# Optimization experiments

Hardware: AMD Instinct MI355X
Metric: run time of the kernel (lower is better)

The kernel has to match this reference:

```python
import jax, jax.numpy as jnp
import numpy as np
from math import factorial

# irreps: list of (multiplicity, l, parity) -- "128x0e + 64x1o + 32x2e"
IRREPS = [(128, 0, 1), (64, 1, -1), (32, 2, 1)]


def _change_basis_real_to_complex(l):
    # e3nn convention: complex SH basis expressed in terms of real SH basis
    q = np.zeros((2 * l + 1, 2 * l + 1), dtype=np.complex128)
    for m in range(-l, 0):
        q[l + m, l + abs(m)] = 1 / np.sqrt(2)
        q[l + m, l - abs(m)] = -1j / np.sqrt(2)
    q[l, l] = 1
    for m in range(1, l + 1):
        q[l + m, l + abs(m)] = (-1) ** m / np.sqrt(2)
        q[l + m, l - abs(m)] = 1j * (-1) ** m / np.sqrt(2)
    return (-1j) ** l * q  # phase makes the real CG coefficients real


def _su2_cg(j1, j2, j3):
    f = factorial
    C = np.zeros((2 * j1 + 1, 2 * j2 + 1, 2 * j3 + 1))
    for m1 in range(-j1, j1 + 1):
        for m2 in range(-j2, j2 + 1):
            m3 = m1 + m2
            if abs(m3) > j3:
                continue
            pref = ((2 * j3 + 1) * f(j3 + j1 - j2) * f(j3 - j1 + j2) * f(j1 + j2 - j3) / f(j1 + j2 + j3 + 1)
                    * f(j3 + m3) * f(j3 - m3) * f(j1 - m1) * f(j1 + m1) * f(j2 - m2) * f(j2 + m2)) ** 0.5
            s = 0.0
            for k in range(0, j1 + j2 - j3 + 1):
                if j1 - m1 - k < 0 or j2 + m2 - k < 0 or j3 - j2 + m1 + k < 0 or j3 - j1 - m2 + k < 0:
                    continue
                s += (-1) ** k / (f(k) * f(j1 + j2 - j3 - k) * f(j1 - m1 - k) * f(j2 + m2 - k)
                                  * f(j3 - j2 + m1 + k) * f(j3 - j1 - m2 + k))
            C[j1 + m1, j2 + m2, j3 + m3] = pref * s
    return C


def _real_cg(l1, l2, l3):
    # real (Wigner-3j style) CG, normalized so sum of squares == 1
    Q1 = _change_basis_real_to_complex(l1)
    Q2 = _change_basis_real_to_complex(l2)
    Q3 = _change_basis_real_to_complex(l3)
    C = _su2_cg(l1, l2, l3).astype(np.complex128)
    C = np.einsum('ij,kl,mn,ikm->jln', Q1, Q2, Q3, C).real
    return (C / np.linalg.norm(C)).astype(np.float32)


def _build_paths():
    paths, fan_in, woff = [], [0] * len(IRREPS), 0
    for i1, (m1, l1, p1) in enumerate(IRREPS):
        for i2, (m2, l2, p2) in enumerate(IRREPS):
            for i3, (m3, l3, p3) in enumerate(IRREPS):
                if p1 * p2 != p3 or not (abs(l1 - l2) <= l3 <= l1 + l2):
                    continue
                paths.append((i1, i2, i3, woff, _real_cg(l1, l2, l3)))
                woff += m1 * m2 * m3
                fan_in[i3] += m1 * m2
    return paths, fan_in, woff

PATHS, FAN_IN, WEIGHT_NUMEL = _build_paths()  # WEIGHT_NUMEL == 4489216
OFFS = np.cumsum([0] + [m * (2 * l + 1) for m, l, _ in IRREPS])  # block offsets (mul_ir layout)
BATCH = 8192


def setup_inputs() -> dict:
    key = jax.random.key(0)
    k1, k2, k3 = jax.random.split(key, 3)
    x1 = jax.random.normal(k1, (BATCH, int(OFFS[-1])), dtype=jnp.float32)
    x2 = jax.random.normal(k2, (BATCH, int(OFFS[-1])), dtype=jnp.float32)
    weight = jax.random.normal(k3, (WEIGHT_NUMEL,), dtype=jnp.float32)
    return {"x1": x1, "x2": x2, "weight": weight}


def reference(x1, x2, weight):
    b = x1.shape[0]
    out_blocks = [jnp.zeros((b, m, 2 * l + 1), dtype=x1.dtype) for m, l, _ in IRREPS]
    for i1, i2, i3, wo, cg in PATHS:
        m1, l1, _ = IRREPS[i1]
        m2, l2, _ = IRREPS[i2]
        m3, l3, _ = IRREPS[i3]
        W = weight[wo:wo + m1 * m2 * m3].reshape(m1, m2, m3)
        xb1 = x1[:, OFFS[i1]:OFFS[i1 + 1]].reshape(b, m1, 2 * l1 + 1)
        xb2 = x2[:, OFFS[i2]:OFFS[i2 + 1]].reshape(b, m2, 2 * l2 + 1)
        # component irrep-norm + element path-norm: sqrt(dim_out / fan_in)
        coeff = np.sqrt((2 * l3 + 1) / FAN_IN[i3]).astype(np.float32)
        out_blocks[i3] = out_blocks[i3] + coeff * jnp.einsum(
            'uvw,bui,bvj,ijk->bwk', W, xb1, xb2, jnp.asarray(cg))
    return jnp.concatenate([ob.reshape(b, -1) for ob in out_blocks], axis=1)
```

## Files before the change

### kernel.cpp

```cpp
#include <hip/hip_runtime.h>
#include <math.h>

#define DIMX 480

typedef float v4f __attribute__((ext_vector_type(4)));
typedef __bf16 v8bf __attribute__((ext_vector_type(8)));
typedef __bf16 v4bf __attribute__((ext_vector_type(4)));

__constant__ int c_pl[11][3] = {
    {0,0,0},{0,1,1},{0,2,2},{1,0,1},{1,1,0},{1,1,2},
    {1,2,1},{2,0,2},{2,1,1},{2,2,0},{2,2,2}};
__constant__ int c_cgoff[11] = {0,1,10,35,44,53,98,143,168,213,238};
__constant__ int c_order[11] = {8,5,0,3,10,4,7,9,6,1,2};

struct cplx { double re, im; };
__device__ inline cplx cmul(cplx a, cplx b) {
    return { a.re*b.re - a.im*b.im, a.re*b.im + a.im*b.re };
}
__device__ double dfact(int n) { double r = 1.0; for (int i = 2; i <= n; ++i) r *= (double)i; return r; }

__device__ double su2cg_elem(int j1, int j2, int j3, int m1, int m2) {
    int m3 = m1 + m2;
    if (m3 < -j3 || m3 > j3) return 0.0;
    double pref = (2.0*j3 + 1.0)
        * dfact(j3 + j1 - j2) * dfact(j3 - j1 + j2) * dfact(j1 + j2 - j3)
        / dfact(j1 + j2 + j3 + 1)
        * dfact(j3 + m3) * dfact(j3 - m3) * dfact(j1 - m1) * dfact(j1 + m1)
        * dfact(j2 - m2) * dfact(j2 + m2);
    pref = sqrt(pref);
    double s = 0.0;
    for (int k = 0; k <= j1 + j2 - j3; ++k) {
        if (j1 - m1 - k < 0 || j2 + m2 - k < 0 ||
            j3 - j2 + m1 + k < 0 || j3 - j1 - m2 + k < 0) continue;
        double d = dfact(k) * dfact(j1 + j2 - j3 - k) * dfact(j1 - m1 - k)
                 * dfact(j2 + m2 - k) * dfact(j3 - j2 + m1 + k) * dfact(j3 - j1 - m2 + k);
        s += ((k & 1) ? -1.0 : 1.0) / d;
    }
    return pref * s;
}

__device__ cplx Qval(int l, int mi, int ri) {
    const double is2 = 0.70710678118654752440;
    int m = mi - l;
    cplx q = {0.0, 0.0};
    if (m < 0) {
        if (ri == l - m)       q = { is2, 0.0 };
        else if (ri == l + m)  q = { 0.0, -is2 };
    } else if (m == 0) {
        if (ri == l)           q = { 1.0, 0.0 };
    } else {
        double s = (m & 1) ? -1.0 : 1.0;
        if (ri == l + m)       q = { s * is2, 0.0 };
        else if (ri == l - m)  q = { 0.0, s * is2 };
    }
    int ph = l & 3;
    cplx r;
    if (ph == 0)      r = q;
    else if (ph == 1) r = {  q.im, -q.re };
    else if (ph == 2) r = { -q.re, -q.im };
    else              r = { -q.im,  q.re };
    return r;
}

__global__ void cg_init_kernel(float* __restrict__ cgout) {
    int p = blockIdx.x;
    int l1 = c_pl[p][0], l2 = c_pl[p][1], l3 = c_pl[p][2];
    int D2 = 2*l2 + 1, D3 = 2*l3 + 1;
    int D = (2*l1 + 1) * D2 * D3;
    int e = threadIdx.x;
    double val = 0.0;
    if (e < D) {
        int j  = e / (D2 * D3);
        int l_ = (e / D3) % D2;
        int n  = e % D3;
        for (int m1 = -l1; m1 <= l1; ++m1)
            for (int m2 = -l2; m2 <= l2; ++m2) {
                int m3 = m1 + m2;
                if (m3 < -l3 || m3 > l3) continue;
                double cgv = su2cg_elem(l1, l2, l3, m1, m2);
                if (cgv == 0.0) continue;
                cplx t = cmul(cmul(Qval(l1, l1 + m1, j), Qval(l2, l2 + m2, l_)),
                              Qval(l3, l3 + m3, n));
                val += t.re * cgv;
            }
    }
    __shared__ double sh[128];
    sh[threadIdx.x] = val * val;
    __syncthreads();
    for (int s = 64; s > 0; s >>= 1) {
        if (threadIdx.x < s) sh[threadIdx.x] += sh[threadIdx.x + s];
        __syncthreads();
    }
    double nrm = sqrt(sh[0]);
    if (e < D) cgout[c_cgoff[p] + e] = (float)(val / nrm);
}

__global__ __launch_bounds__(256) void wt2_kernel(const float* __restrict__ w,
                                                  __bf16* __restrict__ wt2) {
    int c = blockIdx.x * 256 + threadIdx.x;
    int sec, cc;
    if (c < 344064)      { sec = 0; cc = c; }
    else if (c < 507904) { sec = 1; cc = c - 344064; }
    else                 { sec = 2; cc = c - 507904; }
    int l = cc & 15, quad = (cc >> 4) & 3;
    int nblk, kblk, N; size_t soff;
    if (sec == 0)      { nblk = (cc >> 6) & 7; kblk = cc >> 9; N = 128; soff = 0; }
    else if (sec == 1) { nblk = (cc >> 6) & 3; kblk = cc >> 8; N = 64;  soff = 2752512; }
    else               { nblk = (cc >> 6) & 1; kblk = cc >> 7; N = 32;  soff = 4063232; }
    int n = nblk * 16 + l;
    int k = kblk * 32 + quad * 8;
    int rb, pb;
    if (sec == 0) {
        if (k < 16384)      { rb = 0;     pb = 0; }
        else if (k < 20480) { rb = 16384; pb = 3276800; }
        else                { rb = 20480; pb = 4325376; }
    } else if (sec == 1) {
        if (k < 8192)       { rb = 0;     pb = 2097152; }
        else if (k < 16384) { rb = 8192;  pb = 2752512; }
        else if (k < 18432) { rb = 16384; pb = 3932160; }
        else                { rb = 18432; pb = 4194304; }
    } else {
        if (k < 4096)       { rb = 0;     pb = 2621440; }
        else if (k < 8192)  { rb = 4096;  pb = 3801088; }
        else if (k < 12288) { rb = 8192;  pb = 4063232; }
        else                { rb = 12288; pb = 4456448; }
    }
    const float* src = w + pb + (size_t)(k - rb) * N + n;
    v8bf o;
    #pragma unroll
    for (int j = 0; j < 8; ++j) o[j] = (__bf16)src[(size_t)j * N];
    *(v8bf*)(&wt2[soff + (size_t)cc * 8]) = o;
}

static __device__ __forceinline__ void stage_tile(const float* __restrict__ x,
        int b0, int c0, int n4, int S, __bf16* __restrict__ d, int tid) {
    const int cnt = 32 * n4;
    for (int c = tid; c < cnt; c += 256) {
        int row = c / n4, ch = c - row * n4;
        float4 v = *(const float4*)(x + (size_t)(b0 + row) * DIMX + c0 + ch * 4);
        v4bf p;
        p[0] = (__bf16)v.x; p[1] = (__bf16)v.y; p[2] = (__bf16)v.z; p[3] = (__bf16)v.w;
        *(v4bf*)(&d[row * S + ch * 4]) = p;
    }
}

#define XE(A, i) ((float)A[(i) >> 3][(i) & 7])

#define PAIR_REDUCE(NA)                                                  \
    {                                                                    \
        v4f* red_ = (v4f*)xs;                                            \
        __syncthreads();                                                 \
        if (kh) {                                                        \
            _Pragma("unroll")                                            \
            for (int a_ = 0; a_ < (NA); ++a_)                            \
                red_[(rt * 64 + lane) * (NA) + a_] = acc[a_];            \
        }                                                                \
        __syncthreads();                                                 \
        if (!kh) {                                                       \
            _Pragma("unroll")                                            \
            for (int a_ = 0; a_ < (NA); ++a_)                            \
                acc[a_] += red_[(rt * 64 + lane) * (NA) + a_];           \
        }                                                                \
    }

__global__ __launch_bounds__(256, 4) void tp_path(
    const float* __restrict__ x1, const float* __restrict__ x2,
    const __bf16* __restrict__ wt2, const float* __restrict__ cg,
    float* __restrict__ out, float* __restrict__ pa,
    float* __restrict__ pb, float* __restrict__ pc)
{
    __shared__ __align__(16) __bf16 xs[12800];
    const int tid  = threadIdx.x;
    const int lane = tid & 63;
    const int wv   = tid >> 6;
    const int quad = lane >> 4;
    const int l16  = lane & 15;
    const int rt   = wv & 1;
    const int kh   = wv >> 1;
    const int path = c_order[blockIdx.x >> 8];
    const int b0   = (blockIdx.x & 255) * 32;
    const int qil  = (quad * 16 + l16) * 8;
    const int lrow = rt * 16 + l16;

    const float c0n = sqrtf(1.0f / 21504.0f);
    const float c1n = sqrtf(3.0f / 20480.0f);
    const float c2n = sqrtf(5.0f / 13312.0f);

    switch (path) {
    case 0: {
        const int S = 136;
        stage_tile(x1, b0, 0, 32, S, xs, tid);
        stage_tile(x2, b0, 0, 32, S, xs + 32*S, tid);
        __syncthreads();
        const __bf16* X1L = xs + lrow * S;
        const __bf16* X2L = xs + 32*S + lrow * S;
        const float s0 = cg[0] * c0n;
        v4f acc[8];
        #pragma unroll
        for (int c = 0; c < 8; ++c) acc[c] = (v4f)0.f;
        #pragma unroll 1
        for (int u = kh*64; u < kh*64 + 64; ++u) {
            const float s = s0 * (float)X1L[u];
            #pragma unroll 1
            for (int q4 = 0; q4 < 4; ++q4) {
                v8bf xv = *(const v8bf*)(X2L + 32*q4 + quad * 8);
                v8bf af;
                #pragma unroll
                for (int j = 0; j < 8; ++j) af[j] = (__bf16)(s * (float)xv[j]);
                const __bf16* bp = wt2 + (size_t)((u*4 + q4) * 8) * 512 + qil;
                #pragma unroll
                for (int ct = 0; ct < 8; ++ct) {
                    v8bf bf = *(const v8bf*)(bp + ct * 512);
                    acc[ct] = __builtin_amdgcn_mfma_f32_16x16x32_bf16(af, bf, acc[ct], 0, 0, 0);
                }
            }
        }
        PAIR_REDUCE(8)
        if (!kh) {
            #pragma unroll
            for (int i = 0; i < 4; ++i) {
                int r = b0 + rt*16 + quad*4 + i;
                #pragma unroll
                for (int ct = 0; ct < 8; ++ct)
                    out[(size_t)r * DIMX + ct*16 + l16] = acc[ct][i];
            }
        }
        break; }
    case 1: {
        const int S = 200;
        stage_tile(x1, b0, 128, 48, S, xs, tid);
        stage_tile(x2, b0, 128, 48, S, xs + 32*S, tid);
        __syncthreads();
        const __bf16* X1L = xs + lrow * S;
        const __bf16* X2L = xs + 32*S + lrow * S;
        const float d0 = cg[44]*c0n, d1 = cg[48]*c0n, d2 = cg[52]*c0n;
        v4f acc[8];
        #pragma unroll
        for (int c = 0; c < 8; ++c) acc[c] = (v4f)0.f;
        #pragma unroll 1
        for (int tu = kh*32; tu < kh*32 + 32; ++tu) {
            const int u3 = 3 * tu;
            const float m0 = d0*(float)X1L[u3], m1 = d1*(float)X1L[u3+1], m2 = d2*(float)X1L[u3+2];
            #pragma unroll 1
            for (int h = 0; h < 2; ++h) {
                const int col = 96*h + 24*quad;
                v8bf a[3];
                a[0] = *(const v8bf*)(X2L + col);
                a[1] = *(const v8bf*)(X2L + col + 8);
                a[2] = *(const v8bf*)(X2L + col + 16);
                v8bf af;
                #pragma unroll
                for (int j = 0; j < 8; ++j)
                    af[j] = (__bf16)(m0*XE(a,3*j) + m1*XE(a,3*j+1) + m2*XE(a,3*j+2));
                const __bf16* bp = wt2 + (size_t)((512 + tu*2 + h) * 8) * 512 + qil;
                #pragma unroll
                for (int ct = 0; ct < 8; ++ct) {
                    v8bf bf = *(const v8bf*)(bp + ct * 512);
                    acc[ct] = __builtin_amdgcn_mfma_f32_16x16x32_bf16(af, bf, acc[ct], 0, 0, 0);
                }
            }
        }
        PAIR_REDUCE(8)
        if (!kh) {
            #pragma unroll
            for (int i = 0; i < 4; ++i) {
                int r = b0 + rt*16 + quad*4 + i;
                #pragma unroll
                for (int ct = 0; ct < 8; ++ct)
                    pa[(size_t)r * DIMX + ct*16 + l16] = acc[ct][i];
            }
        }
        break; }
    case 2: {
        const int S = 168;
        stage_tile(x1, b0, 320, 40, S, xs, tid);
        stage_tile(x2, b0, 320, 40, S, xs + 32*S, tid);
        __syncthreads();
        const __bf16* X1L = xs + lrow * S;
        const __bf16* X2L = xs + 32*S + lrow * S;
        v4f acc[8];
        #pragma unroll
        for (int c = 0; c < 8; ++c) acc[c] = (v4f)0.f;
        v8bf a[5];
        #pragma unroll
        for (int q = 0; q < 5; ++q) a[q] = *(const v8bf*)(X2L + 40*quad + 8*q);
        #pragma unroll 1
        for (int t = kh*16; t < kh*16 + 16; ++t) {
            const int u5 = 5 * t;
            float m[5];
            #pragma unroll
            for (int kk = 0; kk < 5; ++kk) m[kk] = cg[213+6*kk]*c0n*(float)X1L[u5+kk];
            v8bf af;
            #pragma unroll
            for (int j = 0; j < 8; ++j) {
                float s = 0.f;
                #pragma unroll
                for (int kk = 0; kk < 5; ++kk) s += m[kk] * XE(a, 5*j+kk);
                af[j] = (__bf16)s;
            }
            const __bf16* bp = wt2 + (size_t)((640+t) * 8) * 512 + qil;
            #pragma unroll
            for (int ct = 0; ct < 8; ++ct) {
                v8bf bf = *(const v8bf*)(bp + ct * 512);
                acc[ct] = __builtin_amdgcn_mfma_f32_16x16x32_bf16(af, bf, acc[ct], 0, 0, 0);
            }
        }
        PAIR_REDUCE(8)
        if (!kh) {
            #pragma unroll
            for (int i = 0; i < 4; ++i) {
                int r = b0 + rt*16 + quad*4 + i;
                #pragma unroll
                for (int ct = 0; ct < 8; ++ct)
                    pb[(size_t)r * DIMX + ct*16 + l16] = acc[ct][i];
            }
        }
        break; }
    case 3: {
        const int S1 = 136, S2 = 200;
        stage_tile(x1, b0, 0,   32, S1, xs, tid);
        stage_tile(x2, b0, 128, 48, S2, xs + 32*S1, tid);
        __syncthreads();
        const __bf16* X1L = xs + lrow * S1;
        const __bf16* X2L = xs + 32*S1 + lrow * S2;
        const float g0 = cg[1]*c1n, g1 = cg[5]*c1n, g2 = cg[9]*c1n;
        v4f acc[12];
        #pragma unroll
        for (int c = 0; c < 12; ++c) acc[c] = (v4f)0.f;
        #pragma unroll 1
        for (int tu = kh*64; tu < kh*64 + 64; ++tu) {
            const float xu = (float)X1L[tu];
            const float e0 = g0*xu, e1 = g1*xu, e2 = g2*xu;
            #pragma unroll 1
            for (int h = 0; h < 2; ++h) {
                const int t = tu*2 + h;
                const int col = 96*h + 24*quad;
                v8bf a[3];
                a[0] = *(const v8bf*)(X2L + col);
                a[1] = *(const v8bf*)(X2L + col + 8);
                a[2] = *(const v8bf*)(X2L + col + 16);
                v8bf af[3];
                #pragma unroll
                for (int j = 0; j < 8; ++j) {
                    af[0][j] = (__bf16)(e0 * XE(a, 3*j));
                    af[1][j] = (__bf16)(e1 * XE(a, 3*j+1));
                    af[2][j] = (__bf16)(e2 * XE(a, 3*j+2));
                }
                const __bf16* bp = wt2 + 2752512 + (size_t)(t*4) * 512 + qil;
                #pragma unroll
                for (int cti = 0; cti < 4; ++cti) {
                    v8bf bf = *(const v8bf*)(bp + cti * 512);
                    #pragma unroll
                    for (int p = 0; p < 3; ++p)
                        acc[p*4+cti] = __builtin_amdgcn_mfma_f32_16x16x32_bf16(af[p], bf, acc[p*4+cti], 0, 0, 0);
                }
            }
        }
        PAIR_REDUCE(12)
        if (!kh) {
            #pragma unroll
            for (int i = 0; i < 4; ++i) {
                int r = b0 + rt*16 + quad*4 + i;
                #pragma unroll
                for (int p = 0; p < 3; ++p)
                    #pragma unroll
                    for (int cti = 0; cti < 4; ++cti)
                        pa[(size_t)r * DIMX + 128 + (cti*16 + l16)*3 + p] = acc[p*4+cti][i];
            }
        }
        break; }
    case 4: {
        const int S1 = 200, S2 = 136;
        stage_tile(x1, b0, 128, 48, S1, xs, tid);
        stage_tile(x2, b0, 0,   32, S2, xs + 32*S1, tid);
        __syncthreads();
        const __bf16* X1L = xs + lrow * S1;
        const __bf16* X2L = xs + 32*S1 + lrow * S2;
        const float d0 = cg[35]*c1n, d1 = cg[39]*c1n, d2 = cg[43]*c1n;
        v4f acc[12];
        #pragma unroll
        for (int c = 0; c < 12; ++c) acc[c] = (v4f)0.f;
        #pragma unroll 1
        for (int tu = kh*32; tu < kh*32 + 32; ++tu) {
            const int u3 = 3 * tu;
            const float m0 = d0*(float)X1L[u3], m1 = d1*(float)X1L[u3+1], m2 = d2*(float)X1L[u3+2];
            #pragma unroll 1
            for (int q4 = 0; q4 < 4; ++q4) {
                const int t = tu*4 + q4;
                v8bf xv = *(const v8bf*)(X2L + 32*q4 + quad*8);
                v8bf af[3];
                #pragma unroll
                for (int j = 0; j < 8; ++j) {
                    float x = (float)xv[j];
                    af[0][j] = (__bf16)(m0*x); af[1][j] = (__bf16)(m1*x); af[2][j] = (__bf16)(m2*x);
                }
                const __bf16* bp = wt2 + 2752512 + (size_t)((256+t)*4) * 512 + qil;
                #pragma unroll
                for (int cti = 0; cti < 4; ++cti) {
                    v8bf bf = *(const v8bf*)(bp + cti * 512);
                    #pragma unroll
                    for (int p = 0; p < 3; ++p)
                        acc[p*4+cti] = __builtin_amdgcn_mfma_f32_16x16x32_bf16(af[p], bf, acc[p*4+cti], 0, 0, 0);
                }
            }
        }
        PAIR_REDUCE(12)
        if (!kh) {
            #pragma unroll
            for (int i = 0; i < 4; ++i) {
                int r = b0 + rt*16 + quad*4 + i;
                #pragma unroll
                for (int p = 0; p < 3; ++p)
                    #pragma unroll
                    for (int cti = 0; cti < 4; ++cti)
                        out[(size_t)r * DIMX + 128 + (cti*16 + l16)*3 + p] = acc[p*4+cti][i];
            }
        }
        break; }
    case 5: {
        const int chh = wv >> 1;
        const int S1 = 200, S2 = 168;
        stage_tile(x1, b0, 128, 48, S1, xs, tid);
        stage_tile(x2, b0, 320, 40, S2, xs + 32*S1, tid);
        __syncthreads();
        const __bf16* X1L = xs + lrow * S1;
        const __bf16* X2L = xs + 32*S1 + lrow * S2;
        v4f acc[3][2];
        for (int p = 0; p < 3; ++p) { acc[p][0] = (v4f)0.f; acc[p][1] = (v4f)0.f; }
        #pragma unroll 1
        for (int t = 0; t < 64; ++t) {
            const int u3 = 3 * t;
            float p1[3];
            #pragma unroll
            for (int i1 = 0; i1 < 3; ++i1) p1[i1] = c1n * (float)X1L[u3 + i1];
            float y[5][3];
            #pragma unroll
            for (int j2 = 0; j2 < 5; ++j2)
                #pragma unroll
                for (int p = 0; p < 3; ++p)
                    y[j2][p] = cg[98 + (0*5+j2)*3 + p]*p1[0]
                             + cg[98 + (1*5+j2)*3 + p]*p1[1]
                             + cg[98 + (2*5+j2)*3 + p]*p1[2];
            const int col = 40 * quad;
            v8bf a[5];
            #pragma unroll
            for (int q = 0; q < 5; ++q) a[q] = *(const v8bf*)(X2L + col + 8*q);
            v8bf af[3];
            #pragma unroll
            for (int j = 0; j < 8; ++j) {
                float s0 = 0.f, s1 = 0.f, s2 = 0.f;
                #pragma unroll
                for (int j2 = 0; j2 < 5; ++j2) {
                    float x = XE(a, 5*j + j2);
                    s0 += y[j2][0]*x; s1 += y[j2][1]*x; s2 += y[j2][2]*x;
                }
                af[0][j] = (__bf16)s0; af[1][j] = (__bf16)s1; af[2][j] = (__bf16)s2;
            }
            #pragma unroll
            for (int cti = 0; cti < 2; ++cti) {
                v8bf bf = *(const v8bf*)(wt2 + 2752512 + (size_t)((512+t)*4 + chh*2 + cti)*512 + qil);
                #pragma unroll
                for (int p = 0; p < 3; ++p)
                    acc[p][cti] = __builtin_amdgcn_mfma_f32_16x16x32_bf16(af[p], bf, acc[p][cti], 0, 0, 0);
            }
        }
        #pragma unroll
        for (int i = 0; i < 4; ++i) {
            int r = b0 + rt*16 + quad*4 + i;
            #pragma unroll
            for (int p = 0; p < 3; ++p)
                #pragma unroll
                for (int cti = 0; cti < 2; ++cti)
                    pb[(size_t)r * DIMX + 128 + ((chh*2+cti)*16 + l16)*3 + p] = acc[p][cti][i];
        }
        break; }
    case 6: {
        const int S1 = 168, S2 = 200;
        stage_tile(x1, b0, 320, 40, S1, xs, tid);
        stage_tile(x2, b0, 128, 48, S2, xs + 32*S1, tid);
        __syncthreads();
        const __bf16* X1L = xs + lrow * S1;
        const __bf16* X2L = xs + 32*S1 + lrow * S2;
        v4f acc[12];
        #pragma unroll
        for (int c = 0; c < 12; ++c) acc[c] = (v4f)0.f;
        #pragma unroll 1
        for (int tu = kh*16; tu < kh*16 + 16; ++tu) {
            const int u5 = 5 * tu;
            float p1[5];
            #pragma unroll
            for (int i1 = 0; i1 < 5; ++i1) p1[i1] = c1n * (float)X1L[u5 + i1];
            float y[3][3];
            #pragma unroll
            for (int j2 = 0; j2 < 3; ++j2)
                #pragma unroll
                for (int p = 0; p < 3; ++p) {
                    float s = 0.f;
                    #pragma unroll
                    for (int i1 = 0; i1 < 5; ++i1)
                        s += cg[168 + (i1*3+j2)*3 + p] * p1[i1];
                    y[j2][p] = s;
                }
            #pragma unroll 1
            for (int h = 0; h < 2; ++h) {
                const int t = tu*2 + h;
                const int col = 96*h + 24*quad;
                v8bf a[3];
                a[0] = *(const v8bf*)(X2L + col);
                a[1] = *(const v8bf*)(X2L + col + 8);
                a[2] = *(const v8bf*)(X2L + col + 16);
                v8bf af[3];
                #pragma unroll
                for (int j = 0; j < 8; ++j) {
                    float s0 = 0.f, s1 = 0.f, s2 = 0.f;
                    #pragma unroll
                    for (int j2 = 0; j2 < 3; ++j2) {
                        float x = XE(a, 3*j + j2);
                        s0 += y[j2][0]*x; s1 += y[j2][1]*x; s2 += y[j2][2]*x;
                    }
                    af[0][j] = (__bf16)s0; af[1][j] = (__bf16)s1; af[2][j] = (__bf16)s2;
                }
                const __bf16* bp = wt2 + 2752512 + (size_t)((576+t)*4) * 512 + qil;
                #pragma unroll
                for (int cti = 0; cti < 4; ++cti) {
                    v8bf bf = *(const v8bf*)(bp + cti * 512);
                    #pragma unroll
                    for (int p = 0; p < 3; ++p)
                        acc[p*4+cti] = __builtin_amdgcn_mfma_f32_16x16x32_bf16(af[p], bf, acc[p*4+cti], 0, 0, 0);
                }
            }
        }
        PAIR_REDUCE(12)
        if (!kh) {
            #pragma unroll
            for (int i = 0; i < 4; ++i) {
                int r = b0 + rt*16 + quad*4 + i;
                #pragma unroll
                for (int p = 0; p < 3; ++p)
                    #pragma unroll
                    for (int cti = 0; cti < 4; ++cti)
                        pc[(size_t)r * DIMX + 128 + (cti*16 + l16)*3 + p] = acc[p*4+cti][i];
            }
        }
        break; }
    case 7: {
        const int S1 = 136, S2 = 168;
        stage_tile(x1, b0, 0,   32, S1, xs, tid);
        stage_tile(x2, b0, 320, 40, S2, xs + 32*S1, tid);
        __syncthreads();
        const __bf16* X1L = xs + lrow * S1;
        const __bf16* X2L = xs + 32*S1 + lrow * S2;
        v4f acc[10];
        #pragma unroll
        for (int c = 0; c < 10; ++c) acc[c] = (v4f)0.f;
        v8bf a[5];
        #pragma unroll
        for (int q = 0; q < 5; ++q) a[q] = *(const v8bf*)(X2L + 40*quad + 8*q);
        #pragma unroll 1
        for (int t = kh*64; t < kh*64 + 64; ++t) {
            const float xu = c2n * (float)X1L[t];
            float e[5];
            #pragma unroll
            for (int kk = 0; kk < 5; ++kk) e[kk] = cg[10 + 6*kk] * xu;
            v8bf af[5];
            #pragma unroll
            for (int j = 0; j < 8; ++j)
                #pragma unroll
                for (int kk = 0; kk < 5; ++kk)
                    af[kk][j] = (__bf16)(e[kk] * XE(a, 5*j + kk));
            const __bf16* bp = wt2 + 4063232 + (size_t)(t*2) * 512 + qil;
            #pragma unroll
            for (int cti = 0; cti < 2; ++cti) {
                v8bf bf = *(const v8bf*)(bp + cti * 512);
                #pragma unroll
                for (int kk = 0; kk < 5; ++kk)
                    acc[kk*2+cti] = __builtin_amdgcn_mfma_f32_16x16x32_bf16(af[kk], bf, acc[kk*2+cti], 0, 0, 0);
            }
        }
        PAIR_REDUCE(10)
        if (!kh) {
            #pragma unroll
            for (int i = 0; i < 4; ++i) {
                int r = b0 + rt*16 + quad*4 + i;
                #pragma unroll
                for (int kk = 0; kk < 5; ++kk)
                    #pragma unroll
                    for (int cti = 0; cti < 2; ++cti)
                        pa[(size_t)r * DIMX + 320 + (cti*16 + l16)*5 + kk] = acc[kk*2+cti][i];
            }
        }
        break; }
    case 8: {
        const int S = 200;
        stage_tile(x1, b0, 128, 48, S, xs, tid);
        stage_tile(x2, b0, 128, 48, S, xs + 32*S, tid);
        __syncthreads();
        const __bf16* X1L = xs + lrow * S;
        const __bf16* X2L = xs + 32*S + lrow * S;
        v4f acc[10];
        #pragma unroll
        for (int c = 0; c < 10; ++c) acc[c] = (v4f)0.f;
        #pragma unroll 1
        for (int tu = kh*32; tu < kh*32 + 32; ++tu) {
            const int u3 = 3 * tu;
            float p1[3];
            #pragma unroll
            for (int i1 = 0; i1 < 3; ++i1) p1[i1] = c2n * (float)X1L[u3 + i1];
            float y[3][5];
            #pragma unroll
            for (int j2 = 0; j2 < 3; ++j2)
                #pragma unroll
                for (int kk = 0; kk < 5; ++kk)
                    y[j2][kk] = cg[53 + (0*3+j2)*5 + kk]*p1[0]
                              + cg[53 + (1*3+j2)*5 + kk]*p1[1]
                              + cg[53 + (2*3+j2)*5 + kk]*p1[2];
            #pragma unroll 1
            for (int h = 0; h < 2; ++h) {
                const int t = tu*2 + h;
                const int col = 96*h + 24*quad;
                v8bf a[3];
                a[0] = *(const v8bf*)(X2L + col);
                a[1] = *(const v8bf*)(X2L + col + 8);
                a[2] = *(const v8bf*)(X2L + col + 16);
                v8bf af[5];
                #pragma unroll
                for (int j = 0; j < 8; ++j) {
                    float s[5] = {0.f, 0.f, 0.f, 0.f, 0.f};
                    #pragma unroll
                    for (int j2 = 0; j2 < 3; ++j2) {
                        float x = XE(a, 3*j + j2);
                        #pragma unroll
                        for (int kk = 0; kk < 5; ++kk) s[kk] += y[j2][kk] * x;
                    }
                    #pragma unroll
                    for (int kk = 0; kk < 5; ++kk) af[kk][j] = (__bf16)s[kk];
                }
                const __bf16* bp = wt2 + 4063232 + (size_t)((128+t)*2) * 512 + qil;
                #pragma unroll
                for (int cti = 0; cti < 2; ++cti) {
                    v8bf bf = *(const v8bf*)(bp + cti * 512);
                    #pragma unroll
                    for (int kk = 0; kk < 5; ++kk)
                        acc[kk*2+cti] = __builtin_amdgcn_mfma_f32_16x16x32_bf16(af[kk], bf, acc[kk*2+cti], 0, 0, 0);
                }
            }
        }
        PAIR_REDUCE(10)
        if (!kh) {
            #pragma unroll
            for (int i = 0; i < 4; ++i) {
                int r = b0 + rt*16 + quad*4 + i;
                #pragma unroll
                for (int kk = 0; kk < 5; ++kk)
                    #pragma unroll
                    for (int cti = 0; cti < 2; ++cti)
                        pb[(size_t)r * DIMX + 320 + (cti*16 + l16)*5 + kk] = acc[kk*2+cti][i];
            }
        }
        break; }
    case 9: {
        const int S1 = 168, S2 = 136;
        stage_tile(x1, b0, 320, 40, S1, xs, tid);
        stage_tile(x2, b0, 0,   32, S2, xs + 32*S1, tid);
        __syncthreads();
        const __bf16* X1L = xs + lrow * S1;
        const __bf16* X2L = xs + 32*S1 + lrow * S2;
        v4f acc[10];
        #pragma unroll
        for (int c = 0; c < 10; ++c) acc[c] = (v4f)0.f;
        #pragma unroll 1
        for (int tu = kh*16; tu < kh*16 + 16; ++tu) {
            const int u5 = 5 * tu;
            float m[5];
            #pragma unroll
            for (int kk = 0; kk < 5; ++kk) m[kk] = cg[143 + 6*kk] * c2n * (float)X1L[u5 + kk];
            #pragma unroll 1
            for (int q4 = 0; q4 < 4; ++q4) {
                const int t = tu*4 + q4;
                v8bf xv = *(const v8bf*)(X2L + 32*q4 + quad*8);
                v8bf af[5];
                #pragma unroll
                for (int j = 0; j < 8; ++j) {
                    float x = (float)xv[j];
                    #pragma unroll
                    for (int kk = 0; kk < 5; ++kk) af[kk][j] = (__bf16)(m[kk] * x);
                }
                const __bf16* bp = wt2 + 4063232 + (size_t)((256+t)*2) * 512 + qil;
                #pragma unroll
                for (int cti = 0; cti < 2; ++cti) {
                    v8bf bf = *(const v8bf*)(bp + cti * 512);
                    #pragma unroll
                    for (int kk = 0; kk < 5; ++kk)
                        acc[kk*2+cti] = __builtin_amdgcn_mfma_f32_16x16x32_bf16(af[kk], bf, acc[kk*2+cti], 0, 0, 0);
                }
            }
        }
        PAIR_REDUCE(10)
        if (!kh) {
            #pragma unroll
            for (int i = 0; i < 4; ++i) {
                int r = b0 + rt*16 + quad*4 + i;
                #pragma unroll
                for (int kk = 0; kk < 5; ++kk)
                    #pragma unroll
                    for (int cti = 0; cti < 2; ++cti)
                        out[(size_t)r * DIMX + 320 + (cti*16 + l16)*5 + kk] = acc[kk*2+cti][i];
            }
        }
        break; }
    default: {
        const int chh = wv >> 1;
        const int S = 168;
        stage_tile(x1, b0, 320, 40, S, xs, tid);
        stage_tile(x2, b0, 320, 40, S, xs + 32*S, tid);
        __syncthreads();
        const __bf16* X1L = xs + lrow * S;
        const __bf16* X2L = xs + 32*S + lrow * S;
        v4f acc[5]; for (int p = 0; p < 5; ++p) acc[p] = (v4f)0.f;
        #pragma unroll 1
        for (int t = 0; t < 32; ++t) {
            const int u5 = 5 * t;
            float p1[5];
            #pragma unroll
            for (int i1 = 0; i1 < 5; ++i1) p1[i1] = c2n * (float)X1L[u5 + i1];
            float y[5][5];
            #pragma unroll
            for (int j2 = 0; j2 < 5; ++j2)
                #pragma unroll
                for (int kk = 0; kk < 5; ++kk) {
                    float s = 0.f;
                    #pragma unroll
                    for (int i1 = 0; i1 < 5; ++i1)
                        s += cg[238 + (i1*5+j2)*5 + kk] * p1[i1];
                    y[j2][kk] = s;
                }
            const int col = 40 * quad;
            v8bf a[5];
            #pragma unroll
            for (int q = 0; q < 5; ++q) a[q] = *(const v8bf*)(X2L + col + 8*q);
            v8bf af[5];
            #pragma unroll
            for (int j = 0; j < 8; ++j) {
                float s[5] = {0.f, 0.f, 0.f, 0.f, 0.f};
                #pragma unroll
                for (int j2 = 0; j2 < 5; ++j2) {
                    float x = XE(a, 5*j + j2);
                    #pragma unroll
                    for (int kk = 0; kk < 5; ++kk) s[kk] += y[j2][kk] * x;
                }
                #pragma unroll
                for (int kk = 0; kk < 5; ++kk) af[kk][j] = (__bf16)s[kk];
            }
            v8bf bf = *(const v8bf*)(wt2 + 4063232 + (size_t)((384+t)*2 + chh)*512 + qil);
            #pragma unroll
            for (int kk = 0; kk < 5; ++kk)
                acc[kk] = __builtin_amdgcn_mfma_f32_16x16x32_bf16(af[kk], bf, acc[kk], 0, 0, 0);
        }
        #pragma unroll
        for (int i = 0; i < 4; ++i) {
            int r = b0 + rt*16 + quad*4 + i;
            #pragma unroll
            for (int kk = 0; kk < 5; ++kk)
                pc[(size_t)r * DIMX + 320 + (chh*16 + l16)*5 + kk] = acc[kk][i];
        }
        break; }
    }
}

__global__ void add3_kernel(float4* __restrict__ o, const float4* __restrict__ pa,
                            const float4* __restrict__ pb, const float4* __restrict__ pc) {
    size_t i = (size_t)blockIdx.x * 256 + threadIdx.x;
    int col4 = (int)(i % 120);
    float4 r = o[i], a = pa[i], b = pb[i];
    r.x += a.x + b.x; r.y += a.y + b.y; r.z += a.z + b.z; r.w += a.w + b.w;
    if (col4 >= 32) {
        float4 c = pc[i];
        r.x += c.x; r.y += c.y; r.z += c.z; r.w += c.w;
    }
    o[i] = r;
}

template<bool UW>
__global__ __launch_bounds__(256, 2) void tp_fb(
    const float* __restrict__ x1, const float* __restrict__ x2,
    const float* __restrict__ w, const __bf16* __restrict__ wt2,
    const float* __restrict__ cg, float* __restrict__ out)
{
    __shared__ __bf16 x1s[32 * 488];
    __shared__ __bf16 x2s[32 * 488];
    const int tid  = threadIdx.x;
    const int lane = tid & 63;
    const int wv   = tid >> 6;
    const int quad = lane >> 4;
    const int l16  = lane & 15;
    const int sec  = blockIdx.x % 3;
    const int bt   = blockIdx.x / 3;
    const int b0   = bt * 32;

    for (int c = tid; c < 3840; c += 256) {
        int row = c / 120, ch = c - row * 120;
        float4 v1 = *(const float4*)(x1 + (size_t)(b0 + row) * DIMX + ch * 4);
        float4 v2 = *(const float4*)(x2 + (size_t)(b0 + row) * DIMX + ch * 4);
        v4bf p1, p2;
        p1[0]=(__bf16)v1.x; p1[1]=(__bf16)v1.y; p1[2]=(__bf16)v1.z; p1[3]=(__bf16)v1.w;
        p2[0]=(__bf16)v2.x; p2[1]=(__bf16)v2.y; p2[2]=(__bf16)v2.z; p2[3]=(__bf16)v2.w;
        *(v4bf*)(&x1s[row * 488 + ch * 4]) = p1;
        *(v4bf*)(&x2s[row * 488 + ch * 4]) = p2;
    }
    __syncthreads();

    const int rt  = wv & 1;
    const int chh = wv >> 1;
    const int lrow = rt * 16 + l16;
    const __bf16* X1L = x1s + lrow * 488;
    const __bf16* X2L = x2s + lrow * 488;

    if (sec == 0) {
        const float c0 = sqrtf(1.0f / 21504.0f);
        v4f acc[4];
        #pragma unroll
        for (int b = 0; b < 4; ++b) acc[b] = (v4f)0.f;
        const __bf16* wtw = wt2 + (size_t)(quad * 16 + l16) * 8;
        #pragma unroll 1
        for (int t = 0; t < 336; ++t) {
            const int kt = t * 64;
            v8bf af[2];
            if (kt < 16384) {
                const int u = kt >> 7;
                const float s = cg[0] * c0 * (float)X1L[u];
                #pragma unroll
                for (int ks = 0; ks < 2; ++ks) {
                    v8bf xv = *(const v8bf*)(X2L + (kt & 127) + ks * 32 + quad * 8);
                    #pragma unroll
                    for (int j = 0; j < 8; ++j) af[ks][j] = (__bf16)(s * (float)xv[j]);
                }
            } else if (kt < 20480) {
                const int u = (kt - 16384) >> 6;
                const float m0 = cg[44]*c0*(float)X1L[128+3*u];
                const float m1 = cg[48]*c0*(float)X1L[128+3*u+1];
                const float m2 = cg[52]*c0*(float)X1L[128+3*u+2];
                #pragma unroll
                for (int ks = 0; ks < 2; ++ks) {
                    const int col = 128 + 3 * (ks * 32 + quad * 8);
                    v8bf xv[3];
                    xv[0] = *(const v8bf*)(X2L + col);
                    xv[1] = *(const v8bf*)(X2L + col + 8);
                    xv[2] = *(const v8bf*)(X2L + col + 16);
                    #pragma unroll
                    for (int j = 0; j < 8; ++j)
                        af[ks][j] = (__bf16)(m0*XE(xv,3*j) + m1*XE(xv,3*j+1) + m2*XE(xv,3*j+2));
                }
            } else {
                #pragma unroll
                for (int ks = 0; ks < 2; ++ks) {
                    const int u = ((kt - 20480) >> 5) + ks;
                    float m[5];
                    #pragma unroll
                    for (int k = 0; k < 5; ++k)
                        m[k] = cg[213 + 6*k] * c0 * (float)X1L[320 + 5*u + k];
                    const int col = 320 + 40 * quad;
                    v8bf xv[5];
                    #pragma unroll
                    for (int q = 0; q < 5; ++q) xv[q] = *(const v8bf*)(X2L + col + 8*q);
                    #pragma unroll
                    for (int j = 0; j < 8; ++j) {
                        float a = 0.f;
                        #pragma unroll
                        for (int k = 0; k < 5; ++k) a += m[k] * XE(xv, 5*j+k);
                        af[ks][j] = (__bf16)a;
                    }
                }
            }
            #pragma unroll
            for (int ks = 0; ks < 2; ++ks) {
                const int kblk = (kt >> 5) + ks;
                #pragma unroll
                for (int ct = 0; ct < 4; ++ct) {
                    v8bf bf;
                    if (UW) {
                        bf = *(const v8bf*)(wtw + (size_t)(kblk * 8 + chh * 4 + ct) * 512);
                    } else {
                        int rb, pb;
                        if (kt < 16384)      { rb = 0;     pb = 0; }
                        else if (kt < 20480) { rb = 16384; pb = 3276800; }
                        else                 { rb = 20480; pb = 4325376; }
                        const float* src = w + pb + (size_t)(kt + ks*32 + quad*8 - rb) * 128
                                           + (chh*4 + ct)*16 + l16;
                        #pragma unroll
                        for (int j = 0; j < 8; ++j) bf[j] = (__bf16)src[(size_t)j * 128];
                    }
                    acc[ct] = __builtin_amdgcn_mfma_f32_16x16x32_bf16(af[ks], bf, acc[ct], 0, 0, 0);
                }
            }
        }
        #pragma unroll
        for (int i = 0; i < 4; ++i) {
            const int r = b0 + rt*16 + quad*4 + i;
            float* orow = out + (size_t)r * DIMX;
            #pragma unroll
            for (int ct = 0; ct < 4; ++ct) orow[chh*64 + ct*16 + l16] = acc[ct][i];
        }
    } else if (sec == 1) {
        const float c1 = sqrtf(3.0f / 20480.0f);
        v4f acc[3][2];
        #pragma unroll
        for (int p = 0; p < 3; ++p) { acc[p][0] = (v4f)0.f; acc[p][1] = (v4f)0.f; }
        const __bf16* wtw = wt2 + 2752512 + (size_t)(quad * 16 + l16) * 8;
        #pragma unroll 1
        for (int t = 0; t < 640; ++t) {
            const int kt = t * 32;
            v8bf af[3];
            if (kt < 8192) {
                const int u = kt >> 6;
                const float xv1 = (float)X1L[u];
                const float e0 = cg[1]*c1*xv1, e1 = cg[5]*c1*xv1, e2 = cg[9]*c1*xv1;
                const int col = 128 + 3 * ((kt & 63) + quad * 8);
                v8bf xv[3];
                xv[0] = *(const v8bf*)(X2L + col);
                xv[1] = *(const v8bf*)(X2L + col + 8);
                xv[2] = *(const v8bf*)(X2L + col + 16);
                #pragma unroll
                for (int j = 0; j < 8; ++j) {
                    af[0][j] = (__bf16)(e0 * XE(xv, 3*j));
                    af[1][j] = (__bf16)(e1 * XE(xv, 3*j+1));
                    af[2][j] = (__bf16)(e2 * XE(xv, 3*j+2));
                }
            } else if (kt < 16384) {
                const int q0 = kt - 8192;
                const int u = q0 >> 7;
                const float m0 = cg[35]*c1*(float)X1L[128+3*u];
                const float m1 = cg[39]*c1*(float)X1L[128+3*u+1];
                const float m2 = cg[43]*c1*(float)X1L[128+3*u+2];
                v8bf xv = *(const v8bf*)(X2L + (q0 & 127) + quad * 8);
                #pragma unroll
                for (int j = 0; j < 8; ++j) {
                    float x = (float)xv[j];
                    af[0][j] = (__bf16)(m0 * x);
                    af[1][j] = (__bf16)(m1 * x);
                    af[2][j] = (__bf16)(m2 * x);
                }
            } else if (kt < 18432) {
                const int u = (kt - 16384) >> 5;
                float p1[3];
                #pragma unroll
                for (int i1 = 0; i1 < 3; ++i1) p1[i1] = c1 * (float)X1L[128 + 3*u + i1];
                float y[5][3];
                #pragma unroll
                for (int j2 = 0; j2 < 5; ++j2)
                    #pragma unroll
                    for (int k = 0; k < 3; ++k)
                        y[j2][k] = cg[98 + (0*5+j2)*3 + k]*p1[0]
                                 + cg[98 + (1*5+j2)*3 + k]*p1[1]
                                 + cg[98 + (2*5+j2)*3 + k]*p1[2];
                const int col = 320 + 40 * quad;
                v8bf xv[5];
                #pragma unroll
                for (int q = 0; q < 5; ++q) xv[q] = *(const v8bf*)(X2L + col + 8*q);
                #pragma unroll
                for (int j = 0; j < 8; ++j) {
                    float a0 = 0.f, a1 = 0.f, a2 = 0.f;
                    #pragma unroll
                    for (int j2 = 0; j2 < 5; ++j2) {
                        float x = XE(xv, 5*j + j2);
                        a0 += y[j2][0]*x; a1 += y[j2][1]*x; a2 += y[j2][2]*x;
                    }
                    af[0][j] = (__bf16)a0; af[1][j] = (__bf16)a1; af[2][j] = (__bf16)a2;
                }
            } else {
                const int q0 = kt - 18432;
                const int u = q0 >> 6;
                float p1[5];
                #pragma unroll
                for (int i1 = 0; i1 < 5; ++i1) p1[i1] = c1 * (float)X1L[320 + 5*u + i1];
                float y[3][3];
                #pragma unroll
                for (int j2 = 0; j2 < 3; ++j2)
                    #pragma unroll
                    for (int k = 0; k < 3; ++k) {
                        float s = 0.f;
                        #pragma unroll
                        for (int i1 = 0; i1 < 5; ++i1)
                            s += cg[168 + (i1*3+j2)*3 + k] * p1[i1];
                        y[j2][k] = s;
                    }
                const int col = 128 + 3 * ((q0 & 63) + quad * 8);
                v8bf xv[3];
                xv[0] = *(const v8bf*)(X2L + col);
                xv[1] = *(const v8bf*)(X2L + col + 8);
                xv[2] = *(const v8bf*)(X2L + col + 16);
                #pragma unroll
                for (int j = 0; j < 8; ++j) {
                    float a0 = 0.f, a1 = 0.f, a2 = 0.f;
                    #pragma unroll
                    for (int j2 = 0; j2 < 3; ++j2) {
                        float x = XE(xv, 3*j + j2);
                        a0 += y[j2][0]*x; a1 += y[j2][1]*x; a2 += y[j2][2]*x;
                    }
                    af[0][j] = (__bf16)a0; af[1][j] = (__bf16)a1; af[2][j] = (__bf16)a2;
                }
            }
            #pragma unroll
            for (int cti = 0; cti < 2; ++cti) {
                const int nblk = chh * 2 + cti;
                v8bf bf;
                if (UW) {
                    bf = *(const v8bf*)(wtw + (size_t)(t * 4 + nblk) * 512);
                } else {
                    int rb, pb;
                    if (kt < 8192)       { rb = 0;     pb = 2097152; }
                    else if (kt < 16384) { rb = 8192;  pb = 2752512; }
                    else if (kt < 18432) { rb = 16384; pb = 3932160; }
                    else                 { rb = 18432; pb = 4194304; }
                    const float* src = w + pb + (size_t)(kt + quad*8 - rb) * 64 + nblk*16 + l16;
                    #pragma unroll
                    for (int j = 0; j < 8; ++j) bf[j] = (__bf16)src[(size_t)j * 64];
                }
                #pragma unroll
                for (int p = 0; p < 3; ++p)
                    acc[p][cti] = __builtin_amdgcn_mfma_f32_16x16x32_bf16(af[p], bf, acc[p][cti], 0, 0, 0);
            }
        }
        #pragma unroll
        for (int i = 0; i < 4; ++i) {
            const int r = b0 + rt*16 + quad*4 + i;
            float* orow = out + (size_t)r * DIMX;
            #pragma unroll
            for (int p = 0; p < 3; ++p)
                #pragma unroll
                for (int cti = 0; cti < 2; ++cti)
                    orow[128 + ((chh*2 + cti)*16 + l16) * 3 + p] = acc[p][cti][i];
        }
    } else {
        const float c2 = sqrtf(5.0f / 13312.0f);
        v4f acc[5];
        #pragma unroll
        for (int p = 0; p < 5; ++p) acc[p] = (v4f)0.f;
        const __bf16* wtw = wt2 + 4063232 + (size_t)(quad * 16 + l16) * 8;
        #pragma unroll 1
        for (int t = 0; t < 416; ++t) {
            const int kt = t * 32;
            v8bf af[5];
            if (kt < 4096) {
                const int u = kt >> 5;
                const float s = c2 * (float)X1L[u];
                float e[5];
                #pragma unroll
                for (int k = 0; k < 5; ++k) e[k] = cg[10 + 6*k] * s;
                const int col = 320 + 40 * quad;
                v8bf xv[5];
                #pragma unroll
                for (int q = 0; q < 5; ++q) xv[q] = *(const v8bf*)(X2L + col + 8*q);
                #pragma unroll
                for (int j = 0; j < 8; ++j)
                    #pragma unroll
                    for (int k = 0; k < 5; ++k)
                        af[k][j] = (__bf16)(e[k] * XE(xv, 5*j + k));
            } else if (kt < 8192) {
                const int q0 = kt - 4096;
                const int u = q0 >> 6;
                float p1[3];
                #pragma unroll
                for (int i1 = 0; i1 < 3; ++i1) p1[i1] = c2 * (float)X1L[128 + 3*u + i1];
                float y[3][5];
                #pragma unroll
                for (int j2 = 0; j2 < 3; ++j2)
                    #pragma unroll
                    for (int k = 0; k < 5; ++k)
                        y[j2][k] = cg[53 + (0*3+j2)*5 + k]*p1[0]
                                 + cg[53 + (1*3+j2)*5 + k]*p1[1]
                                 + cg[53 + (2*3+j2)*5 + k]*p1[2];
                const int col = 128 + 3 * ((q0 & 63) + quad * 8);
                v8bf xv[3];
                xv[0] = *(const v8bf*)(X2L + col);
                xv[1] = *(const v8bf*)(X2L + col + 8);
                xv[2] = *(const v8bf*)(X2L + col + 16);
                #pragma unroll
                for (int j = 0; j < 8; ++j) {
                    float a[5] = {0.f, 0.f, 0.f, 0.f, 0.f};
                    #pragma unroll
                    for (int j2 = 0; j2 < 3; ++j2) {
                        float x = XE(xv, 3*j + j2);
                        #pragma unroll
                        for (int k = 0; k < 5; ++k) a[k] += y[j2][k] * x;
                    }
                    #pragma unroll
                    for (int k = 0; k < 5; ++k) af[k][j] = (__bf16)a[k];
                }
            } else if (kt < 12288) {
                const int q0 = kt - 8192;
                const int u = q0 >> 7;
                float m[5];
                #pragma unroll
                for (int k = 0; k < 5; ++k)
                    m[k] = cg[143 + 6*k] * c2 * (float)X1L[320 + 5*u + k];
                v8bf xv = *(const v8bf*)(X2L + (q0 & 127) + quad * 8);
                #pragma unroll
                for (int j = 0; j < 8; ++j) {
                    float x = (float)xv[j];
                    #pragma unroll
                    for (int k = 0; k < 5; ++k) af[k][j] = (__bf16)(m[k] * x);
                }
            } else {
                const int u = (kt - 12288) >> 5;
                float p1[5];
                #pragma unroll
                for (int i1 = 0; i1 < 5; ++i1) p1[i1] = c2 * (float)X1L[320 + 5*u + i1];
                float y[5][5];
                #pragma unroll
                for (int j2 = 0; j2 < 5; ++j2)
                    #pragma unroll
                    for (int k = 0; k < 5; ++k) {
                        float s = 0.f;
                        #pragma unroll
                        for (int i1 = 0; i1 < 5; ++i1)
                            s += cg[238 + (i1*5+j2)*5 + k] * p1[i1];
                        y[j2][k] = s;
                    }
                const int col = 320 + 40 * quad;
                v8bf xv[5];
                #pragma unroll
                for (int q = 0; q < 5; ++q) xv[q] = *(const v8bf*)(X2L + col + 8*q);
                #pragma unroll
                for (int j = 0; j < 8; ++j) {
                    float a[5] = {0.f, 0.f, 0.f, 0.f, 0.f};
                    #pragma unroll
                    for (int j2 = 0; j2 < 5; ++j2) {
                        float x = XE(xv, 5*j + j2);
                        #pragma unroll
                        for (int k = 0; k < 5; ++k) a[k] += y[j2][k] * x;
                    }
                    #pragma unroll
                    for (int k = 0; k < 5; ++k) af[k][j] = (__bf16)a[k];
                }
            }
            {
                v8bf bf;
                if (UW) {
                    bf = *(const v8bf*)(wtw + (size_t)(t * 2 + chh) * 512);
                } else {
                    int rb, pb;
                    if (kt < 4096)       { rb = 0;     pb = 2621440; }
                    else if (kt < 8192)  { rb = 4096;  pb = 3801088; }
                    else if (kt < 12288) { rb = 8192;  pb = 4063232; }
                    else                 { rb = 12288; pb = 4456448; }
                    const float* src = w + pb + (size_t)(kt + quad*8 - rb) * 32 + chh*16 + l16;
                    #pragma unroll
                    for (int j = 0; j < 8; ++j) bf[j] = (__bf16)src[(size_t)j * 32];
                }
                #pragma unroll
                for (int k = 0; k < 5; ++k)
                    acc[k] = __builtin_amdgcn_mfma_f32_16x16x32_bf16(af[k], bf, acc[k], 0, 0, 0);
            }
        }
        #pragma unroll
        for (int i = 0; i < 4; ++i) {
            const int r = b0 + rt*16 + quad*4 + i;
            float* orow = out + (size_t)r * DIMX;
            #pragma unroll
            for (int k = 0; k < 5; ++k)
                orow[320 + (chh*16 + l16) * 5 + k] = acc[k][i];
        }
    }
}

extern "C" void kernel_launch(void* const* d_in, const int* in_sizes, int n_in,
                              void* d_out, int out_size, void* d_ws, size_t ws_size,
                              hipStream_t stream) {
    const float* x1 = (const float*)d_in[0];
    const float* x2 = (const float*)d_in[1];
    const float* wt_f = (const float*)d_in[2];
    float* out = (float*)d_out;
    (void)in_sizes; (void)n_in; (void)out_size;

    const size_t WT_BYTES = (size_t)4489216 * 2;
    const size_t CG_PAD   = 4096;
    const size_t PART     = (size_t)8192 * DIMX * 4;
    const size_t PA_OFF   = WT_BYTES + CG_PAD;
    const size_t NEED     = PA_OFF + 3 * PART;

    float*  cgp = (float*)((char*)d_ws + WT_BYTES);
    __bf16* wtp = (__bf16*)d_ws;
    float*  pa  = (float*)((char*)d_ws + PA_OFF);
    float*  pb  = (float*)((char*)d_ws + PA_OFF + PART);
    float*  pc  = (float*)((char*)d_ws + PA_OFF + 2 * PART);

    if (ws_size >= NEED) {
        cg_init_kernel<<<dim3(11), dim3(128), 0, stream>>>(cgp);
        wt2_kernel<<<dim3(2192), dim3(256), 0, stream>>>(wt_f, wtp);
        tp_path<<<dim3(2816), dim3(256), 0, stream>>>(x1, x2, wtp, cgp, out, pa, pb, pc);
        add3_kernel<<<dim3(3840), dim3(256), 0, stream>>>(
            (float4*)out, (const float4*)pa, (const float4*)pb, (const float4*)pc);
    } else if (ws_size >= WT_BYTES + CG_PAD) {
        cg_init_kernel<<<dim3(11), dim3(128), 0, stream>>>(cgp);
        wt2_kernel<<<dim3(2192), dim3(256), 0, stream>>>(wt_f, wtp);
        tp_fb<true><<<dim3(768), dim3(256), 0, stream>>>(x1, x2, wt_f, wtp, cgp, out);
    } else {
        float* cgs = (float*)d_ws;
        cg_init_kernel<<<dim3(11), dim3(128), 0, stream>>>(cgs);
        tp_fb<false><<<dim3(768), dim3(256), 0, stream>>>(x1, x2, wt_f, (const __bf16*)d_ws, cgs, out);
    }
}
```

Before: 382.9 us.

## Split path 0 across two blocks and build CG coefficients on host

Path 0 (the heaviest 128x128x128 path) is split into two launch slots, each doing half the u range, with the second half writing to the pc partial buffer. The grid grows from 2816 to 3072 blocks and the launch order is rebalanced. add3 now always adds pc, which also removes a branch. CG coefficients are computed once on the host and copied over with hipMemcpyAsync instead of running an init kernel each call. The rewritten add3 assumes every pc column, including the first 128 that nothing else writes, is valid, so the split path must fully cover them.

```diff
diff --git a/kernel.cpp b/kernel.cpp
--- a/kernel.cpp
+++ b/kernel.cpp
@@ -7,42 +7,38 @@
 typedef __bf16 v8bf __attribute__((ext_vector_type(8)));
 typedef __bf16 v4bf __attribute__((ext_vector_type(4)));
 
-__constant__ int c_pl[11][3] = {
-    {0,0,0},{0,1,1},{0,2,2},{1,0,1},{1,1,0},{1,1,2},
-    {1,2,1},{2,0,2},{2,1,1},{2,2,0},{2,2,2}};
-__constant__ int c_cgoff[11] = {0,1,10,35,44,53,98,143,168,213,238};
-__constant__ int c_order[11] = {8,5,0,3,10,4,7,9,6,1,2};
-
-struct cplx { double re, im; };
-__device__ inline cplx cmul(cplx a, cplx b) {
+__constant__ int c_order[12] = {8,5,10,3,4,7,9,0,11,6,1,2};
+
+struct hcplx { double re, im; };
+static inline hcplx hcmul(hcplx a, hcplx b) {
     return { a.re*b.re - a.im*b.im, a.re*b.im + a.im*b.re };
 }
-__device__ double dfact(int n) { double r = 1.0; for (int i = 2; i <= n; ++i) r *= (double)i; return r; }
-
-__device__ double su2cg_elem(int j1, int j2, int j3, int m1, int m2) {
+static double hdfact(int n) { double r = 1.0; for (int i = 2; i <= n; ++i) r *= (double)i; return r; }
+
+static double hsu2cg(int j1, int j2, int j3, int m1, int m2) {
     int m3 = m1 + m2;
     if (m3 < -j3 || m3 > j3) return 0.0;
     double pref = (2.0*j3 + 1.0)
-        * dfact(j3 + j1 - j2) * dfact(j3 - j1 + j2) * dfact(j1 + j2 - j3)
-        / dfact(j1 + j2 + j3 + 1)
-        * dfact(j3 + m3) * dfact(j3 - m3) * dfact(j1 - m1) * dfact(j1 + m1)
-        * dfact(j2 - m2) * dfact(j2 + m2);
+        * hdfact(j3 + j1 - j2) * hdfact(j3 - j1 + j2) * hdfact(j1 + j2 - j3)
+        / hdfact(j1 + j2 + j3 + 1)
+        * hdfact(j3 + m3) * hdfact(j3 - m3) * hdfact(j1 - m1) * hdfact(j1 + m1)
+        * hdfact(j2 - m2) * hdfact(j2 + m2);
     pref = sqrt(pref);
     double s = 0.0;
     for (int k = 0; k <= j1 + j2 - j3; ++k) {
         if (j1 - m1 - k < 0 || j2 + m2 - k < 0 ||
             j3 - j2 + m1 + k < 0 || j3 - j1 - m2 + k < 0) continue;
-        double d = dfact(k) * dfact(j1 + j2 - j3 - k) * dfact(j1 - m1 - k)
-                 * dfact(j2 + m2 - k) * dfact(j3 - j2 + m1 + k) * dfact(j3 - j1 - m2 + k);
+        double d = hdfact(k) * hdfact(j1 + j2 - j3 - k) * hdfact(j1 - m1 - k)
+                 * hdfact(j2 + m2 - k) * hdfact(j3 - j2 + m1 + k) * hdfact(j3 - j1 - m2 + k);
         s += ((k & 1) ? -1.0 : 1.0) / d;
     }
     return pref * s;
 }
 
-__device__ cplx Qval(int l, int mi, int ri) {
+static hcplx hQval(int l, int mi, int ri) {
     const double is2 = 0.70710678118654752440;
     int m = mi - l;
-    cplx q = {0.0, 0.0};
+    hcplx q = {0.0, 0.0};
     if (m < 0) {
         if (ri == l - m)       q = { is2, 0.0 };
         else if (ri == l + m)  q = { 0.0, -is2 };
@@ -54,7 +50,7 @@
         else if (ri == l - m)  q = { 0.0, s * is2 };
     }
     int ph = l & 3;
-    cplx r;
+    hcplx r;
     if (ph == 0)      r = q;
     else if (ph == 1) r = {  q.im, -q.re };
     else if (ph == 2) r = { -q.re, -q.im };
@@ -62,37 +58,37 @@
     return r;
 }
 
-__global__ void cg_init_kernel(float* __restrict__ cgout) {
-    int p = blockIdx.x;
-    int l1 = c_pl[p][0], l2 = c_pl[p][1], l3 = c_pl[p][2];
-    int D2 = 2*l2 + 1, D3 = 2*l3 + 1;
-    int D = (2*l1 + 1) * D2 * D3;
-    int e = threadIdx.x;
-    double val = 0.0;
-    if (e < D) {
-        int j  = e / (D2 * D3);
-        int l_ = (e / D3) % D2;
-        int n  = e % D3;
-        for (int m1 = -l1; m1 <= l1; ++m1)
-            for (int m2 = -l2; m2 <= l2; ++m2) {
-                int m3 = m1 + m2;
-                if (m3 < -l3 || m3 > l3) continue;
-                double cgv = su2cg_elem(l1, l2, l3, m1, m2);
-                if (cgv == 0.0) continue;
-                cplx t = cmul(cmul(Qval(l1, l1 + m1, j), Qval(l2, l2 + m2, l_)),
-                              Qval(l3, l3 + m3, n));
-                val += t.re * cgv;
-            }
+static void build_cg_host(float* cgout) {
+    static const int pl[11][3] = {
+        {0,0,0},{0,1,1},{0,2,2},{1,0,1},{1,1,0},{1,1,2},
+        {1,2,1},{2,0,2},{2,1,1},{2,2,0},{2,2,2}};
+    static const int cgo[11] = {0,1,10,35,44,53,98,143,168,213,238};
+    for (int p = 0; p < 11; ++p) {
+        int l1 = pl[p][0], l2 = pl[p][1], l3 = pl[p][2];
+        int D2 = 2*l2 + 1, D3 = 2*l3 + 1;
+        int D = (2*l1 + 1) * D2 * D3;
+        double vals[125];
+        double ss = 0.0;
+        for (int e = 0; e < D; ++e) {
+            int j  = e / (D2 * D3);
+            int l_ = (e / D3) % D2;
+            int n  = e % D3;
+            double val = 0.0;
+            for (int m1 = -l1; m1 <= l1; ++m1)
+                for (int m2 = -l2; m2 <= l2; ++m2) {
+                    int m3 = m1 + m2;
+                    if (m3 < -l3 || m3 > l3) continue;
+                    double cgv = hsu2cg(l1, l2, l3, m1, m2);
+                    if (cgv == 0.0) continue;
+                    hcplx t = hcmul(hcmul(hQval(l1, l1 + m1, j), hQval(l2, l2 + m2, l_)),
+                                    hQval(l3, l3 + m3, n));
+                    val += t.re * cgv;
+                }
+            vals[e] = val; ss += val * val;
+        }
+        double nrm = sqrt(ss);
+        for (int e = 0; e < D; ++e) cgout[cgo[p] + e] = (float)(vals[e] / nrm);
     }
-    __shared__ double sh[128];
-    sh[threadIdx.x] = val * val;
-    __syncthreads();
-    for (int s = 64; s > 0; s >>= 1) {
-        if (threadIdx.x < s) sh[threadIdx.x] += sh[threadIdx.x + s];
-        __syncthreads();
-    }
-    double nrm = sqrt(sh[0]);
-    if (e < D) cgout[c_cgoff[p] + e] = (float)(val / nrm);
 }
 
 __global__ __launch_bounds__(256) void wt2_kernel(const float* __restrict__ w,
@@ -187,7 +183,9 @@
     const float c2n = sqrtf(5.0f / 13312.0f);
 
     switch (path) {
-    case 0: {
+    case 0: case 11: {
+        float* __restrict__ dst = (path == 0) ? out : pc;
+        const int ub = ((path == 11) ? 64 : 0) + kh * 32;
         const int S = 136;
         stage_tile(x1, b0, 0, 32, S, xs, tid);
         stage_tile(x2, b0, 0, 32, S, xs + 32*S, tid);
@@ -199,9 +197,9 @@
         #pragma unroll
         for (int c = 0; c < 8; ++c) acc[c] = (v4f)0.f;
         #pragma unroll 1
-        for (int u = kh*64; u < kh*64 + 64; ++u) {
+        for (int u = ub; u < ub + 32; ++u) {
             const float s = s0 * (float)X1L[u];
-            #pragma unroll 1
+            #pragma unroll 2
             for (int q4 = 0; q4 < 4; ++q4) {
                 v8bf xv = *(const v8bf*)(X2L + 32*q4 + quad * 8);
                 v8bf af;
@@ -222,7 +220,7 @@
                 int r = b0 + rt*16 + quad*4 + i;
                 #pragma unroll
                 for (int ct = 0; ct < 8; ++ct)
-                    out[(size_t)r * DIMX + ct*16 + l16] = acc[ct][i];
+                    dst[(size_t)r * DIMX + ct*16 + l16] = acc[ct][i];
             }
         }
         break; }
@@ -770,13 +768,9 @@
 __global__ void add3_kernel(float4* __restrict__ o, const float4* __restrict__ pa,
                             const float4* __restrict__ pb, const float4* __restrict__ pc) {
     size_t i = (size_t)blockIdx.x * 256 + threadIdx.x;
-    int col4 = (int)(i % 120);
-    float4 r = o[i], a = pa[i], b = pb[i];
-    r.x += a.x + b.x; r.y += a.y + b.y; r.z += a.z + b.z; r.w += a.w + b.w;
-    if (col4 >= 32) {
-        float4 c = pc[i];
-        r.x += c.x; r.y += c.y; r.z += c.z; r.w += c.w;
-    }
+    float4 r = o[i], a = pa[i], b = pb[i], c = pc[i];
+    r.x += a.x + b.x + c.x; r.y += a.y + b.y + c.y;
+    r.z += a.z + b.z + c.z; r.w += a.w + b.w + c.w;
     o[i] = r;
 }
 
@@ -1172,6 +1166,10 @@
     float* out = (float*)d_out;
     (void)in_sizes; (void)n_in; (void)out_size;
 
+    static float h_cg[363];
+    static bool h_cg_done = false;
+    if (!h_cg_done) { build_cg_host(h_cg); h_cg_done = true; }
+
     const size_t WT_BYTES = (size_t)4489216 * 2;
     const size_t CG_PAD   = 4096;
     const size_t PART     = (size_t)8192 * DIMX * 4;
@@ -1185,18 +1183,18 @@
     float*  pc  = (float*)((char*)d_ws + PA_OFF + 2 * PART);
 
     if (ws_size >= NEED) {
-        cg_init_kernel<<<dim3(11), dim3(128), 0, stream>>>(cgp);
+        hipMemcpyAsync(cgp, h_cg, sizeof(h_cg), hipMemcpyHostToDevice, stream);
         wt2_kernel<<<dim3(2192), dim3(256), 0, stream>>>(wt_f, wtp);
-        tp_path<<<dim3(2816), dim3(256), 0, stream>>>(x1, x2, wtp, cgp, out, pa, pb, pc);
+        tp_path<<<dim3(3072), dim3(256), 0, stream>>>(x1, x2, wtp, cgp, out, pa, pb, pc);
         add3_kernel<<<dim3(3840), dim3(256), 0, stream>>>(
             (float4*)out, (const float4*)pa, (const float4*)pb, (const float4*)pc);
     } else if (ws_size >= WT_BYTES + CG_PAD) {
-        cg_init_kernel<<<dim3(11), dim3(128), 0, stream>>>(cgp);
+        hipMemcpyAsync(cgp, h_cg, sizeof(h_cg), hipMemcpyHostToDevice, stream);
         wt2_kernel<<<dim3(2192), dim3(256), 0, stream>>>(wt_f, wtp);
         tp_fb<true><<<dim3(768), dim3(256), 0, stream>>>(x1, x2, wt_f, wtp, cgp, out);
     } else {
         float* cgs = (float*)d_ws;
-        cg_init_kernel<<<dim3(11), dim3(128), 0, stream>>>(cgs);
+        hipMemcpyAsync(cgs, h_cg, sizeof(h_cg), hipMemcpyHostToDevice, stream);
         tp_fb<false><<<dim3(768), dim3(256), 0, stream>>>(x1, x2, wt_f, (const __bf16*)d_ws, cgs, out);
     }
 }
```

After: 337.4 us. 11.9% less time.
